# Performance work log

Hardware: AMD Instinct MI355X
Metric: run time of the kernel (lower is better)

Reference implementation:

```python
import jax, jax.numpy as jnp
import numpy as np

B, S, D, MAX_LEN = 8, 2048, 512, 2048
NEG_INF = jnp.float32(-jnp.inf)


def setup_inputs() -> dict:
    key = jax.random.key(0)
    ks = jax.random.split(key, 10)
    s = 1.0 / np.sqrt(D)
    inp = {
        "x": jax.random.normal(ks[0], (B, S, D), dtype=jnp.float32),
        "pos_table": jax.random.normal(ks[1], (MAX_LEN, D), dtype=jnp.float32) * 0.02,
        "Wq": jax.random.normal(ks[2], (D, D), dtype=jnp.float32) * s,
        "bq": jnp.zeros((D,), dtype=jnp.float32),
        "Wk": jax.random.normal(ks[3], (D, D), dtype=jnp.float32) * s,
        "bk": jnp.zeros((D,), dtype=jnp.float32),
        "Wv": jax.random.normal(ks[4], (D, D), dtype=jnp.float32) * s,
        "bv": jnp.zeros((D,), dtype=jnp.float32),
        "Wd": jax.random.normal(ks[5], (D, D), dtype=jnp.float32) * s,
        "bd": jnp.zeros((D,), dtype=jnp.float32),
    }
    return inp


def reference(x, pos_table, Wq, bq, Wk, bk, Wv, bv, Wd, bd):
    # add learned positional embeddings (add_pos=True path): arange over seq dim
    x = x + pos_table[:x.shape[-2]]  # [B,S,D]
    # torch nn.Linear: y = x @ W.T + b
    q = jnp.einsum("bsd,ed->bse", x, Wq) + bq
    k = jnp.einsum("bsd,ed->bse", x, Wk) + bk
    v = jnp.einsum("bsd,ed->bse", x, Wv) + bv
    v = jnp.where(jnp.isnan(v), 0.0, v)  # nan_to_num(nan=0)
    scale = 1.0 / jnp.sqrt(jnp.float32(D))
    scores = jnp.einsum("bqd,bkd->bqk", q, k) * scale  # [B,S,S]
    scores = jnp.where(jnp.isnan(scores), NEG_INF, scores)  # nan_to_num(nan=-inf)
    attn = jax.nn.softmax(scores, axis=2)
    y = jnp.einsum("bqk,bkd->bqd", attn, v)
    return jnp.einsum("bsd,ed->bse", y, Wd) + bd
```

## Files before the change

### kernel.cpp

```cpp
#include <hip/hip_runtime.h>
#include <stdint.h>

typedef __bf16 bf16x8 __attribute__((ext_vector_type(8)));
typedef float f32x4 __attribute__((ext_vector_type(4)));

static constexpr float QK_SCALE = 0.044194173824159216f;

__device__ __forceinline__ uint16_t f2bf(float f) {
    uint32_t x = __builtin_bit_cast(uint32_t, f);
    x += 0x7FFFu + ((x >> 16) & 1u);
    return (uint16_t)(x >> 16);
}

__device__ __forceinline__ void cp16(const uint16_t* g, uint16_t* l) {
    __builtin_amdgcn_global_load_lds(
        (__attribute__((address_space(1))) void*)(uint16_t*)g,
        (__attribute__((address_space(3))) void*)l,
        16, 0, 0);
}

template <int MODE>
__global__ __launch_bounds__(256, 3) void gemm_nt(
    const uint16_t* __restrict__ A, const uint16_t* __restrict__ Bm,
    void* __restrict__ C0, void* __restrict__ C1, void* __restrict__ C2,
    const float* __restrict__ bias0, const float* __restrict__ bias1,
    const float* __restrict__ bias2,
    float scale, int K, int ldc, long bsA, long bsB, long bsC,
    int scols, int stPerBatch)
{
    __shared__ __align__(16) uint16_t SH[3][8192];

    const uint32_t id  = blockIdx.x;
    const uint32_t xcd = id & 7u;
    const uint32_t p   = id >> 3;
    const uint32_t q   = p >> 4;
    const uint32_t w   = p & 15u;
    const uint32_t g   = q * 8u + xcd;
    const uint32_t bz  = g / (uint32_t)stPerBatch;
    const uint32_t gs  = g - bz * (uint32_t)stPerBatch;
    const uint32_t sr  = gs / (uint32_t)scols;
    const uint32_t sc  = gs - sr * (uint32_t)scols;
    const int bm = (int)(sr * 4u + (w >> 2));
    const int bn = (int)(sc * 4u + (w & 3u));

    const int t  = threadIdx.x;
    const int wave = t >> 6, lane = t & 63;
    const int wm = (wave >> 1) * 64, wn = (wave & 1) * 64;
    const int lm = lane & 15, lq = lane >> 4;
    const int sw = lq ^ ((lm >> 1) & 3);

    const uint16_t* Ab = A  + (long)bz * bsA + (long)bm * 128 * K;
    const uint16_t* Bb = Bm + (long)bz * bsB + (long)bn * 128 * K;

    long goff[2]; int loff[2];
#pragma unroll
    for (int j = 0; j < 2; ++j) {
        const int s  = j * 256 + t;
        const int r  = s >> 2;
        const int cs = s & 3;
        const int cg = cs ^ ((r >> 1) & 3);
        goff[j] = (long)r * K + cg * 8;
        loff[j] = s * 8;
    }

    const int KI = K >> 5;

#pragma unroll
    for (int st = 0; st < 2; ++st)
#pragma unroll
        for (int j = 0; j < 2; ++j) {
            cp16(Ab + goff[j] + st * 32, SH[st] + loff[j]);
            cp16(Bb + goff[j] + st * 32, SH[st] + 4096 + loff[j]);
        }

    f32x4 acc[4][4] = {};
    float rsum[4] = {0.f, 0.f, 0.f, 0.f};

    int cur = 0, pf = 2;
    for (int k = 0; k < KI; ++k) {
        asm volatile("s_waitcnt vmcnt(4) lgkmcnt(0)\n\ts_barrier" ::: "memory");

        int kp = k + 2; if (kp >= KI) kp = KI - 1;
        uint16_t* dst = SH[pf];
        const long ko = (long)kp * 32;
#pragma unroll
        for (int j = 0; j < 2; ++j) {
            cp16(Ab + goff[j] + ko, dst + loff[j]);
            cp16(Bb + goff[j] + ko, dst + 4096 + loff[j]);
        }

        const uint16_t* buf = SH[cur];
        bf16x8 af[4], bfr[4];
#pragma unroll
        for (int i = 0; i < 4; ++i)
            af[i]  = *(const bf16x8*)&buf[((wm + i * 16 + lm) * 4 + sw) * 8];
#pragma unroll
        for (int i = 0; i < 4; ++i)
            bfr[i] = *(const bf16x8*)&buf[4096 + ((wn + i * 16 + lm) * 4 + sw) * 8];

        if (MODE == 5) {
#pragma unroll
            for (int j = 0; j < 4; ++j) {
                const uint4 u = __builtin_bit_cast(uint4, af[j]);
                float s0 = __builtin_bit_cast(float, u.x << 16)
                         + __builtin_bit_cast(float, u.x & 0xFFFF0000u);
                float s1 = __builtin_bit_cast(float, u.y << 16)
                         + __builtin_bit_cast(float, u.y & 0xFFFF0000u);
                float s2 = __builtin_bit_cast(float, u.z << 16)
                         + __builtin_bit_cast(float, u.z & 0xFFFF0000u);
                float s3 = __builtin_bit_cast(float, u.w << 16)
                         + __builtin_bit_cast(float, u.w & 0xFFFF0000u);
                rsum[j] += (s0 + s1) + (s2 + s3);
            }
        }

#pragma unroll
        for (int i = 0; i < 4; ++i)
#pragma unroll
            for (int j = 0; j < 4; ++j)
                acc[i][j] = __builtin_amdgcn_mfma_f32_16x16x32_bf16(
                    bfr[i], af[j], acc[i][j], 0, 0, 0);

        cur = (cur == 2) ? 0 : cur + 1;
        pf  = (pf  == 2) ? 0 : pf  + 1;
    }

    float inv[4];
    if (MODE == 5) {
#pragma unroll
        for (int j = 0; j < 4; ++j) {
            float s = rsum[j];
            s += __shfl_xor(s, 16);
            s += __shfl_xor(s, 32);
            inv[j] = 1.f / s;
        }
    }

    const int mb = bm * 128 + wm + lm;
    const int nb = bn * 128 + wn + lq * 4;
#pragma unroll
    for (int i = 0; i < 4; ++i) {
        const int n = nb + i * 16;
        if (MODE == 0 || MODE == 5) {
#pragma unroll
            for (int j = 0; j < 4; ++j) {
                const int m = mb + j * 16;
                float v0, v1, v2, v3;
                if (MODE == 5) {
                    v0 = acc[i][j][0] * inv[j];
                    v1 = acc[i][j][1] * inv[j];
                    v2 = acc[i][j][2] * inv[j];
                    v3 = acc[i][j][3] * inv[j];
                } else {
                    v0 = acc[i][j][0] * scale;
                    v1 = acc[i][j][1] * scale;
                    v2 = acc[i][j][2] * scale;
                    v3 = acc[i][j][3] * scale;
                }
                const uint32_t lo = (uint32_t)f2bf(v0) | ((uint32_t)f2bf(v1) << 16);
                const uint32_t hi = (uint32_t)f2bf(v2) | ((uint32_t)f2bf(v3) << 16);
                *(uint2*)&((uint16_t*)C0)[(long)bz * bsC + (long)m * ldc + n] =
                    make_uint2(lo, hi);
            }
        } else if (MODE == 2) {
            const float4 b4 = *(const float4*)&bias0[n];
#pragma unroll
            for (int j = 0; j < 4; ++j) {
                const int m = mb + j * 16;
                *(float4*)&((float*)C0)[(long)m * ldc + n] = make_float4(
                    acc[i][j][0] + b4.x, acc[i][j][1] + b4.y,
                    acc[i][j][2] + b4.z, acc[i][j][3] + b4.w);
            }
        } else {
            const int sec = n >> 9, nn = n & 511;
            const float* bp = sec == 0 ? bias0 : (sec == 1 ? bias1 : bias2);
            const float4 b4 = *(const float4*)&bp[nn];
#pragma unroll
            for (int j = 0; j < 4; ++j) {
                const int m = mb + j * 16;
                if (sec < 2) {
                    uint16_t* Cq = (uint16_t*)(sec == 0 ? C0 : C1);
                    const uint32_t lo = (uint32_t)f2bf(acc[i][j][0] + b4.x) |
                                        ((uint32_t)f2bf(acc[i][j][1] + b4.y) << 16);
                    const uint32_t hi = (uint32_t)f2bf(acc[i][j][2] + b4.z) |
                                        ((uint32_t)f2bf(acc[i][j][3] + b4.w) << 16);
                    *(uint2*)&Cq[(long)m * 512 + nn] = make_uint2(lo, hi);
                } else {
                    const int bb = m >> 11, ss = m & 2047;
                    uint16_t* vt = (uint16_t*)C2 + ((long)bb * 512 + nn) * 2048 + ss;
                    vt[0]        = f2bf(acc[i][j][0] + b4.x);
                    vt[2048]     = f2bf(acc[i][j][1] + b4.y);
                    vt[2 * 2048] = f2bf(acc[i][j][2] + b4.z);
                    vt[3 * 2048] = f2bf(acc[i][j][3] + b4.w);
                }
            }
        }
    }
}

template <int MODE>
__global__ __launch_bounds__(512, 2) void gemm_nt8(
    const uint16_t* __restrict__ A, const uint16_t* __restrict__ Bm,
    void* __restrict__ C0,
    float scale, int K, int ldc, long bsA, long bsB, long bsC,
    int scols, int stPerBatch)
{
    __shared__ __align__(16) uint16_t SH[3][16384];

    const uint32_t id  = blockIdx.x;
    const uint32_t xcd = id & 7u;
    const uint32_t p   = id >> 3;
    const uint32_t q   = p >> 4;
    const uint32_t w   = p & 15u;
    const uint32_t g   = q * 8u + xcd;
    const uint32_t bz  = g / (uint32_t)stPerBatch;
    const uint32_t gs  = g - bz * (uint32_t)stPerBatch;
    const uint32_t sr  = gs / (uint32_t)scols;
    const uint32_t sc  = gs - sr * (uint32_t)scols;
    const int bm = (int)(sr * 4u + (w >> 2));
    const int bn = (int)(sc * 4u + (w & 3u));

    const int t  = threadIdx.x;
    const int wave = t >> 6, lane = t & 63;
    const int wm2 = (wave >> 2) * 128;
    const int wn2 = (wave & 3) * 64;
    const int lm = lane & 15, lq = lane >> 4;
    const int sw = lq ^ ((lm >> 1) & 3);

    const uint16_t* Ab = A  + (long)bz * bsA + (long)bm * 256 * K;
    const uint16_t* Bb = Bm + (long)bz * bsB + (long)bn * 256 * K;

    long goff[2]; int loff[2];
#pragma unroll
    for (int j = 0; j < 2; ++j) {
        const int s  = j * 512 + t;
        const int r  = s >> 2;
        const int cs = s & 3;
        const int cg = cs ^ ((r >> 1) & 3);
        goff[j] = (long)r * K + cg * 8;
        loff[j] = s * 8;
    }

    const int KI = K >> 5;

#pragma unroll
    for (int st = 0; st < 2; ++st)
#pragma unroll
        for (int j = 0; j < 2; ++j) {
            cp16(Ab + goff[j] + st * 32, SH[st] + loff[j]);
            cp16(Bb + goff[j] + st * 32, SH[st] + 8192 + loff[j]);
        }

    f32x4 acc[4][8] = {};

    int cur = 0, pf = 2;
    for (int k = 0; k < KI; ++k) {
        asm volatile("s_waitcnt vmcnt(4) lgkmcnt(0)\n\ts_barrier" ::: "memory");

        int kp = k + 2; if (kp >= KI) kp = KI - 1;
        uint16_t* dst = SH[pf];
        const long ko = (long)kp * 32;
#pragma unroll
        for (int j = 0; j < 2; ++j) {
            cp16(Ab + goff[j] + ko, dst + loff[j]);
            cp16(Bb + goff[j] + ko, dst + 8192 + loff[j]);
        }

        const uint16_t* buf = SH[cur];
        bf16x8 af[8], bfr[4];
#define RDA(jj) (*(const bf16x8*)&buf[((wm2 + (jj) * 16 + lm) * 4 + sw) * 8])
#define RDB(ii) (*(const bf16x8*)&buf[8192 + ((wn2 + (ii) * 16 + lm) * 4 + sw) * 8])
        bfr[0] = RDB(0); bfr[1] = RDB(1); bfr[2] = RDB(2); bfr[3] = RDB(3);
        af[0] = RDA(0); af[1] = RDA(1); af[2] = RDA(2); af[3] = RDA(3);
        af[4] = RDA(4); af[5] = RDA(5); af[6] = RDA(6); af[7] = RDA(7);
#pragma unroll
        for (int pp = 0; pp < 4; ++pp) {
            __builtin_amdgcn_s_setprio(1);
#pragma unroll
            for (int i = 0; i < 4; ++i) {
                acc[i][2 * pp]     = __builtin_amdgcn_mfma_f32_16x16x32_bf16(
                    bfr[i], af[2 * pp],     acc[i][2 * pp],     0, 0, 0);
                acc[i][2 * pp + 1] = __builtin_amdgcn_mfma_f32_16x16x32_bf16(
                    bfr[i], af[2 * pp + 1], acc[i][2 * pp + 1], 0, 0, 0);
            }
            __builtin_amdgcn_s_setprio(0);
        }
#undef RDA
#undef RDB

        cur = (cur == 2) ? 0 : cur + 1;
        pf  = (pf  == 2) ? 0 : pf  + 1;
    }

    const int mb = bm * 256 + wm2 + lm;
    const int nb = bn * 256 + wn2 + lq * 4;
#pragma unroll
    for (int j = 0; j < 8; ++j) {
        const int m = mb + j * 16;
#pragma unroll
        for (int i = 0; i < 4; ++i) {
            const int n = nb + i * 16;
            float v0, v1, v2, v3;
            if (MODE == 4) {
                v0 = __expf(acc[i][j][0] * scale);
                v1 = __expf(acc[i][j][1] * scale);
                v2 = __expf(acc[i][j][2] * scale);
                v3 = __expf(acc[i][j][3] * scale);
            } else {
                v0 = acc[i][j][0] * scale; v1 = acc[i][j][1] * scale;
                v2 = acc[i][j][2] * scale; v3 = acc[i][j][3] * scale;
            }
            const uint32_t lo = (uint32_t)f2bf(v0) | ((uint32_t)f2bf(v1) << 16);
            const uint32_t hi = (uint32_t)f2bf(v2) | ((uint32_t)f2bf(v3) << 16);
            *(uint2*)&((uint16_t*)C0)[(long)bz * bsC + (long)m * ldc + n] =
                make_uint2(lo, hi);
        }
    }
}

__global__ __launch_bounds__(256) void prep_x(const float* __restrict__ x,
                                              const float* __restrict__ pos,
                                              uint16_t* __restrict__ xb)
{
    const long i8 = ((long)blockIdx.x * 256 + threadIdx.x) * 8;
    const long p8 = i8 & ((1l << 20) - 1);
    const float4* xv = (const float4*)(x + i8);
    const float4* pv = (const float4*)(pos + p8);
    const float4 a0 = xv[0], a1 = xv[1];
    const float4 b0 = pv[0], b1 = pv[1];
    uint16_t o[8];
    o[0] = f2bf(a0.x + b0.x); o[1] = f2bf(a0.y + b0.y);
    o[2] = f2bf(a0.z + b0.z); o[3] = f2bf(a0.w + b0.w);
    o[4] = f2bf(a1.x + b1.x); o[5] = f2bf(a1.y + b1.y);
    o[6] = f2bf(a1.z + b1.z); o[7] = f2bf(a1.w + b1.w);
    *(uint4*)(xb + i8) = *(uint4*)o;
}

__global__ __launch_bounds__(256) void prep_w(
    const float* __restrict__ Wq, const float* __restrict__ Wk,
    const float* __restrict__ Wv, const float* __restrict__ Wd,
    uint16_t* __restrict__ wqkv, uint16_t* __restrict__ wd)
{
    const long f = ((long)blockIdx.x * 256 + threadIdx.x) * 8;
    const int  w = (int)(f >> 18);
    const long off = f & 262143;
    const float* src = (w == 0) ? Wq : (w == 1) ? Wk : (w == 2) ? Wv : Wd;
    uint16_t* dst = (w < 3) ? (wqkv + (long)w * 262144 + off) : (wd + off);
    const float4* s4 = (const float4*)(src + off);
    const float4 a = s4[0], b = s4[1];
    uint16_t o[8];
    o[0] = f2bf(a.x); o[1] = f2bf(a.y); o[2] = f2bf(a.z); o[3] = f2bf(a.w);
    o[4] = f2bf(b.x); o[5] = f2bf(b.y); o[6] = f2bf(b.z); o[7] = f2bf(b.w);
    *(uint4*)dst = *(uint4*)o;
}

extern "C" void kernel_launch(void* const* d_in, const int* in_sizes, int n_in,
                              void* d_out, int out_size, void* d_ws, size_t ws_size,
                              hipStream_t stream)
{
    const float* x   = (const float*)d_in[0];
    const float* pos = (const float*)d_in[1];
    const float* Wq  = (const float*)d_in[2];
    const float* bq  = (const float*)d_in[3];
    const float* Wk  = (const float*)d_in[4];
    const float* bk  = (const float*)d_in[5];
    const float* Wv  = (const float*)d_in[6];
    const float* bv  = (const float*)d_in[7];
    const float* Wd  = (const float*)d_in[8];
    const float* bd  = (const float*)d_in[9];
    float* out = (float*)d_out;

    char* ws = (char*)d_ws;
    uint16_t* xb   = (uint16_t*)(ws);
    uint16_t* wqkv = (uint16_t*)(ws + 16777216);
    uint16_t* wd   = (uint16_t*)(ws + 18350080);
    uint16_t* Qb   = (uint16_t*)(ws + 18874368);
    uint16_t* Kb   = (uint16_t*)(ws + 35651584);
    uint16_t* Vt   = (uint16_t*)(ws + 52428800);
    uint16_t* Pb   = (uint16_t*)(ws + 69206016);
    uint16_t* yb   = (uint16_t*)(ws + 136314880);

    prep_x<<<4096, 256, 0, stream>>>(x, pos, xb);
    prep_w<<<512, 256, 0, stream>>>(Wq, Wk, Wv, Wd, wqkv, wd);

    gemm_nt<3><<<1536, 256, 0, stream>>>(
        xb, wqkv, Qb, Kb, Vt, bq, bk, bv, 1.0f, 512, 512, 0, 0, 0, 3, 96);

    gemm_nt8<4><<<512, 512, 0, stream>>>(
        Qb, Kb, Pb, QK_SCALE, 512, 2048, (long)2048 * 512, (long)2048 * 512,
        (long)2048 * 2048, 2, 4);

    gemm_nt<5><<<512, 256, 0, stream>>>(
        Pb, Vt, yb, nullptr, nullptr, nullptr, nullptr, nullptr,
        1.0f, 2048, 512, (long)2048 * 2048, (long)512 * 2048,
        (long)2048 * 512, 1, 4);

    gemm_nt<2><<<512, 256, 0, stream>>>(
        yb, wd, out, nullptr, nullptr, bd, nullptr, nullptr,
        1.0f, 512, 512, 0, 0, 0, 1, 32);
}
```

Baseline: 263.7 us.

## Compute softmax row sums in QK epilogue and use smaller-tile PV/output GEMMs

The QK^T kernel now accumulates exp row sums in fp32 during its epilogue and atomically adds them into a rowsum buffer. This replaces the per-k-step bf16 unpacking and summation that the PV GEMM previously did. A new gemm_pv kernel with 64x128 tiles and 1024 blocks handles both the normalized PV product and the output projection, raising block count and occupancy. In exchange it adds atomics, a memset, and reuses the start of the workspace (the xb region) for rowsum, which is safe only because xb is dead after the QKV GEMM.

```diff
diff --git a/kernel.cpp b/kernel.cpp
--- a/kernel.cpp
+++ b/kernel.cpp
@@ -74,7 +74,6 @@
         }
 
     f32x4 acc[4][4] = {};
-    float rsum[4] = {0.f, 0.f, 0.f, 0.f};
 
     int cur = 0, pf = 2;
     for (int k = 0; k < KI; ++k) {
@@ -98,22 +97,6 @@
         for (int i = 0; i < 4; ++i)
             bfr[i] = *(const bf16x8*)&buf[4096 + ((wn + i * 16 + lm) * 4 + sw) * 8];
 
-        if (MODE == 5) {
-#pragma unroll
-            for (int j = 0; j < 4; ++j) {
-                const uint4 u = __builtin_bit_cast(uint4, af[j]);
-                float s0 = __builtin_bit_cast(float, u.x << 16)
-                         + __builtin_bit_cast(float, u.x & 0xFFFF0000u);
-                float s1 = __builtin_bit_cast(float, u.y << 16)
-                         + __builtin_bit_cast(float, u.y & 0xFFFF0000u);
-                float s2 = __builtin_bit_cast(float, u.z << 16)
-                         + __builtin_bit_cast(float, u.z & 0xFFFF0000u);
-                float s3 = __builtin_bit_cast(float, u.w << 16)
-                         + __builtin_bit_cast(float, u.w & 0xFFFF0000u);
-                rsum[j] += (s0 + s1) + (s2 + s3);
-            }
-        }
-
 #pragma unroll
         for (int i = 0; i < 4; ++i)
 #pragma unroll
@@ -125,51 +108,21 @@
         pf  = (pf  == 2) ? 0 : pf  + 1;
     }
 
-    float inv[4];
-    if (MODE == 5) {
-#pragma unroll
-        for (int j = 0; j < 4; ++j) {
-            float s = rsum[j];
-            s += __shfl_xor(s, 16);
-            s += __shfl_xor(s, 32);
-            inv[j] = 1.f / s;
-        }
-    }
-
     const int mb = bm * 128 + wm + lm;
     const int nb = bn * 128 + wn + lq * 4;
 #pragma unroll
     for (int i = 0; i < 4; ++i) {
         const int n = nb + i * 16;
-        if (MODE == 0 || MODE == 5) {
+        if (MODE == 0) {
 #pragma unroll
             for (int j = 0; j < 4; ++j) {
                 const int m = mb + j * 16;
-                float v0, v1, v2, v3;
-                if (MODE == 5) {
-                    v0 = acc[i][j][0] * inv[j];
-                    v1 = acc[i][j][1] * inv[j];
-                    v2 = acc[i][j][2] * inv[j];
-                    v3 = acc[i][j][3] * inv[j];
-                } else {
-                    v0 = acc[i][j][0] * scale;
-                    v1 = acc[i][j][1] * scale;
-                    v2 = acc[i][j][2] * scale;
-                    v3 = acc[i][j][3] * scale;
-                }
-                const uint32_t lo = (uint32_t)f2bf(v0) | ((uint32_t)f2bf(v1) << 16);
-                const uint32_t hi = (uint32_t)f2bf(v2) | ((uint32_t)f2bf(v3) << 16);
+                const uint32_t lo = (uint32_t)f2bf(acc[i][j][0] * scale) |
+                                    ((uint32_t)f2bf(acc[i][j][1] * scale) << 16);
+                const uint32_t hi = (uint32_t)f2bf(acc[i][j][2] * scale) |
+                                    ((uint32_t)f2bf(acc[i][j][3] * scale) << 16);
                 *(uint2*)&((uint16_t*)C0)[(long)bz * bsC + (long)m * ldc + n] =
                     make_uint2(lo, hi);
-            }
-        } else if (MODE == 2) {
-            const float4 b4 = *(const float4*)&bias0[n];
-#pragma unroll
-            for (int j = 0; j < 4; ++j) {
-                const int m = mb + j * 16;
-                *(float4*)&((float*)C0)[(long)m * ldc + n] = make_float4(
-                    acc[i][j][0] + b4.x, acc[i][j][1] + b4.y,
-                    acc[i][j][2] + b4.z, acc[i][j][3] + b4.w);
             }
         } else {
             const int sec = n >> 9, nn = n & 511;
@@ -201,7 +154,7 @@
 template <int MODE>
 __global__ __launch_bounds__(512, 2) void gemm_nt8(
     const uint16_t* __restrict__ A, const uint16_t* __restrict__ Bm,
-    void* __restrict__ C0,
+    void* __restrict__ C0, float* __restrict__ rowsum,
     float scale, int K, int ldc, long bsA, long bsB, long bsC,
     int scols, int stPerBatch)
 {
@@ -297,23 +250,138 @@
 #pragma unroll
     for (int j = 0; j < 8; ++j) {
         const int m = mb + j * 16;
+        float rsj = 0.f;
 #pragma unroll
         for (int i = 0; i < 4; ++i) {
             const int n = nb + i * 16;
-            float v0, v1, v2, v3;
-            if (MODE == 4) {
-                v0 = __expf(acc[i][j][0] * scale);
-                v1 = __expf(acc[i][j][1] * scale);
-                v2 = __expf(acc[i][j][2] * scale);
-                v3 = __expf(acc[i][j][3] * scale);
-            } else {
-                v0 = acc[i][j][0] * scale; v1 = acc[i][j][1] * scale;
-                v2 = acc[i][j][2] * scale; v3 = acc[i][j][3] * scale;
-            }
+            const float v0 = __expf(acc[i][j][0] * scale);
+            const float v1 = __expf(acc[i][j][1] * scale);
+            const float v2 = __expf(acc[i][j][2] * scale);
+            const float v3 = __expf(acc[i][j][3] * scale);
+            rsj += (v0 + v1) + (v2 + v3);
             const uint32_t lo = (uint32_t)f2bf(v0) | ((uint32_t)f2bf(v1) << 16);
             const uint32_t hi = (uint32_t)f2bf(v2) | ((uint32_t)f2bf(v3) << 16);
             *(uint2*)&((uint16_t*)C0)[(long)bz * bsC + (long)m * ldc + n] =
                 make_uint2(lo, hi);
+        }
+        rsj += __shfl_xor(rsj, 16);
+        rsj += __shfl_xor(rsj, 32);
+        if (lq == 0)
+            atomicAdd(&rowsum[(long)bz * 2048 + m], rsj);
+    }
+}
+
+template <int MODE>
+__global__ __launch_bounds__(256, 4) void gemm_pv(
+    const uint16_t* __restrict__ A, const uint16_t* __restrict__ Bm,
+    void* __restrict__ C0, const float* __restrict__ aux,
+    int K, int ldc, long bsA, long bsB, long bsC,
+    int scols, int stPerBatch)
+{
+    __shared__ __align__(16) uint16_t SH[3][6144];
+
+    const uint32_t id  = blockIdx.x;
+    const uint32_t xcd = id & 7u;
+    const uint32_t p   = id >> 3;
+    const uint32_t q   = p >> 4;
+    const uint32_t w   = p & 15u;
+    const uint32_t g   = q * 8u + xcd;
+    const uint32_t bz  = g / (uint32_t)stPerBatch;
+    const uint32_t gs  = g - bz * (uint32_t)stPerBatch;
+    const uint32_t sr  = gs / (uint32_t)scols;
+    const uint32_t sc  = gs - sr * (uint32_t)scols;
+    const int bm = (int)(sr * 4u + (w >> 2));
+    const int bn = (int)(sc * 4u + (w & 3u));
+
+    const int t  = threadIdx.x;
+    const int wave = t >> 6, lane = t & 63;
+    const int wm = (wave >> 1) * 32, wn = (wave & 1) * 64;
+    const int lm = lane & 15, lq = lane >> 4;
+    const int sw = lq ^ ((lm >> 1) & 3);
+
+    const uint16_t* Ab = A  + (long)bz * bsA + (long)bm * 64 * K;
+    const uint16_t* Bb = Bm + (long)bz * bsB + (long)bn * 128 * K;
+
+    const int rA  = t >> 2, csA = t & 3;
+    const int cgA = csA ^ ((rA >> 1) & 3);
+    const long goffA = (long)rA * K + cgA * 8;
+    const int  loffA = t * 8;
+    long goffB[2]; int loffB[2];
+#pragma unroll
+    for (int j = 0; j < 2; ++j) {
+        const int s  = j * 256 + t;
+        const int r  = s >> 2;
+        const int cs = s & 3;
+        const int cg = cs ^ ((r >> 1) & 3);
+        goffB[j] = (long)r * K + cg * 8;
+        loffB[j] = 2048 + s * 8;
+    }
+
+    const int KI = K >> 5;
+
+#pragma unroll
+    for (int st = 0; st < 2; ++st) {
+        cp16(Ab + goffA + st * 32, SH[st] + loffA);
+        cp16(Bb + goffB[0] + st * 32, SH[st] + loffB[0]);
+        cp16(Bb + goffB[1] + st * 32, SH[st] + loffB[1]);
+    }
+
+    f32x4 acc[4][2] = {};
+
+    int cur = 0, pf = 2;
+    for (int k = 0; k < KI; ++k) {
+        asm volatile("s_waitcnt vmcnt(3) lgkmcnt(0)\n\ts_barrier" ::: "memory");
+
+        int kp = k + 2; if (kp >= KI) kp = KI - 1;
+        uint16_t* dst = SH[pf];
+        const long ko = (long)kp * 32;
+        cp16(Ab + goffA + ko, dst + loffA);
+        cp16(Bb + goffB[0] + ko, dst + loffB[0]);
+        cp16(Bb + goffB[1] + ko, dst + loffB[1]);
+
+        const uint16_t* buf = SH[cur];
+        bf16x8 af[2], bfr[4];
+#pragma unroll
+        for (int j = 0; j < 2; ++j)
+            af[j]  = *(const bf16x8*)&buf[((wm + j * 16 + lm) * 4 + sw) * 8];
+#pragma unroll
+        for (int i = 0; i < 4; ++i)
+            bfr[i] = *(const bf16x8*)&buf[2048 + ((wn + i * 16 + lm) * 4 + sw) * 8];
+
+#pragma unroll
+        for (int i = 0; i < 4; ++i)
+#pragma unroll
+            for (int j = 0; j < 2; ++j)
+                acc[i][j] = __builtin_amdgcn_mfma_f32_16x16x32_bf16(
+                    bfr[i], af[j], acc[i][j], 0, 0, 0);
+
+        cur = (cur == 2) ? 0 : cur + 1;
+        pf  = (pf  == 2) ? 0 : pf  + 1;
+    }
+
+    const int mb = bm * 64 + wm + lm;
+    const int nb = bn * 128 + wn + lq * 4;
+#pragma unroll
+    for (int j = 0; j < 2; ++j) {
+        const int m = mb + j * 16;
+        float inv;
+        if (MODE == 6) inv = 1.f / aux[(long)bz * 2048 + m];
+#pragma unroll
+        for (int i = 0; i < 4; ++i) {
+            const int n = nb + i * 16;
+            if (MODE == 6) {
+                const uint32_t lo = (uint32_t)f2bf(acc[i][j][0] * inv) |
+                                    ((uint32_t)f2bf(acc[i][j][1] * inv) << 16);
+                const uint32_t hi = (uint32_t)f2bf(acc[i][j][2] * inv) |
+                                    ((uint32_t)f2bf(acc[i][j][3] * inv) << 16);
+                *(uint2*)&((uint16_t*)C0)[(long)bz * bsC + (long)m * ldc + n] =
+                    make_uint2(lo, hi);
+            } else {
+                const float4 b4 = *(const float4*)&aux[n];
+                *(float4*)&((float*)C0)[(long)m * ldc + n] = make_float4(
+                    acc[i][j][0] + b4.x, acc[i][j][1] + b4.y,
+                    acc[i][j][2] + b4.z, acc[i][j][3] + b4.w);
+            }
         }
     }
 }
@@ -379,6 +447,7 @@
     uint16_t* Vt   = (uint16_t*)(ws + 52428800);
     uint16_t* Pb   = (uint16_t*)(ws + 69206016);
     uint16_t* yb   = (uint16_t*)(ws + 136314880);
+    float* rowsum = (float*)ws;
 
     prep_x<<<4096, 256, 0, stream>>>(x, pos, xb);
     prep_w<<<512, 256, 0, stream>>>(Wq, Wk, Wv, Wd, wqkv, wd);
@@ -386,16 +455,16 @@
     gemm_nt<3><<<1536, 256, 0, stream>>>(
         xb, wqkv, Qb, Kb, Vt, bq, bk, bv, 1.0f, 512, 512, 0, 0, 0, 3, 96);
 
+    hipMemsetAsync(rowsum, 0, 16384 * sizeof(float), stream);
+
     gemm_nt8<4><<<512, 512, 0, stream>>>(
-        Qb, Kb, Pb, QK_SCALE, 512, 2048, (long)2048 * 512, (long)2048 * 512,
-        (long)2048 * 2048, 2, 4);
-
-    gemm_nt<5><<<512, 256, 0, stream>>>(
-        Pb, Vt, yb, nullptr, nullptr, nullptr, nullptr, nullptr,
-        1.0f, 2048, 512, (long)2048 * 2048, (long)512 * 2048,
-        (long)2048 * 512, 1, 4);
-
-    gemm_nt<2><<<512, 256, 0, stream>>>(
-        yb, wd, out, nullptr, nullptr, bd, nullptr, nullptr,
-        1.0f, 512, 512, 0, 0, 0, 1, 32);
-}
+        Qb, Kb, Pb, rowsum, QK_SCALE, 512, 2048, (long)2048 * 512,
+        (long)2048 * 512, (long)2048 * 2048, 2, 4);
+
+    gemm_pv<6><<<1024, 256, 0, stream>>>(
+        Pb, Vt, yb, rowsum, 2048, 512, (long)2048 * 2048, (long)512 * 2048,
+        (long)2048 * 512, 1, 8);
+
+    gemm_pv<2><<<1024, 256, 0, stream>>>(
+        yb, wd, out, bd, 512, 512, 0, 0, 0, 1, 64);
+}
```

New measurement: 296.1 us. 1.12x slower.
